# Kernel tuning notes

Measured on AMD Instinct MI355X. Metric: run time of the kernel, lower is better.

The kernel has to match this reference:

```python
import jax, jax.numpy as jnp
import numpy as np
import math

HIDDEN = 1024
Q_SIZE = 1024
KV_SIZE = 1024
OUT_SIZE = 1024
N_HEADS = 16
D_K = HIDDEN // N_HEADS


def setup_inputs() -> dict:
    key = jax.random.key(0)
    ks = jax.random.split(key, 9)
    b, s, t = 8, 2048, 512
    sc = 0.02
    return {
        "hiddens": jax.random.normal(ks[0], (b, s, KV_SIZE), jnp.float32),
        "query_hiddens": jax.random.normal(ks[1], (b, t, Q_SIZE), jnp.float32),
        "mask": jax.random.randint(ks[2], (b, s), 0, 2, jnp.int32),
        "W_q": jax.random.normal(ks[3], (Q_SIZE, HIDDEN), jnp.float32) * sc,
        "b_q": jnp.zeros((HIDDEN,), jnp.float32),
        "W_k": jax.random.normal(ks[4], (KV_SIZE, HIDDEN), jnp.float32) * sc,
        "W_v": jax.random.normal(ks[5], (KV_SIZE, HIDDEN), jnp.float32) * sc,
        "W_o": jax.random.normal(ks[6], (HIDDEN, OUT_SIZE), jnp.float32) * sc,
        "b_o": jnp.zeros((OUT_SIZE,), jnp.float32),
    }


def reference(hiddens, query_hiddens, mask, W_q, b_q, W_k, W_v, W_o, b_o):
    b, t, _ = query_hiddens.shape
    s = hiddens.shape[1]
    # projections (dropout p=0 in eval -> identity)
    Q = (query_hiddens @ W_q + b_q).reshape(b, t, N_HEADS, D_K)
    K = (hiddens @ W_k).reshape(b, s, N_HEADS, D_K)
    V = (hiddens @ W_v).reshape(b, s, N_HEADS, D_K)
    # scores: [b, t, s, h] matching e = (Q*K).sum(-1)/sqrt(d_k)
    e = jnp.einsum('bthd,bshd->btsh', Q, K) / math.sqrt(D_K)
    neg = (1.0 - mask.astype(e.dtype)) * (-1e20)  # [b, s]
    e = e + neg[:, None, :, None]
    a = jax.nn.softmax(e, axis=2)  # softmax over seqlen
    concat = jnp.einsum('btsh,bshd->bthd', a, V).reshape(b, t, HIDDEN)
    context = concat @ W_o + b_o
    return context, a.mean(axis=-1)
```

## Files before the change

### kernel.cpp

```cpp
#include <hip/hip_runtime.h>
#include <hip/hip_bf16.h>

using short8 = __attribute__((ext_vector_type(8))) short;
using f32x4  = __attribute__((ext_vector_type(4))) float;

#define LSK 72

#define GLDS(gptr, lptr) __builtin_amdgcn_global_load_lds( \
    (const __attribute__((address_space(1))) void*)(gptr), \
    (__attribute__((address_space(3))) void*)(lptr), 16, 0, 0)

static __device__ __forceinline__ short f2b(float f) {
    unsigned u = __builtin_bit_cast(unsigned, f);
    unsigned r = (u + 0x7fffu + ((u >> 16) & 1u)) >> 16;
    return (short)r;
}

__global__ void cvt_bf16(const float* __restrict__ in, short* __restrict__ out, int n) {
    int i = (blockIdx.x * 256 + threadIdx.x) * 4;
    if (i >= n) return;
    float4 v = *(const float4*)(in + i);
    short4 o = make_short4(f2b(v.x), f2b(v.y), f2b(v.z), f2b(v.w));
    *(short4*)(out + i) = o;
}

__global__ void cvt_t4(const float* __restrict__ W0, const float* __restrict__ W1,
                       const float* __restrict__ W2, const float* __restrict__ W3,
                       short* __restrict__ Wt0) {
    __shared__ short tile[32][33];
    const float* Ws[4] = {W0, W1, W2, W3};
    const float* W = Ws[blockIdx.z];
    short* Wt = Wt0 + (size_t)blockIdx.z * 1024 * 1024;
    const int K = 1024, N = 1024;
    int n0 = blockIdx.x * 32, k0 = blockIdx.y * 32;
    int tx = threadIdx.x, ty = threadIdx.y;
#pragma unroll
    for (int i = 0; i < 4; i++) {
        int r = ty + i * 8;
        tile[r][tx] = f2b(W[(size_t)(k0 + r) * N + n0 + tx]);
    }
    __syncthreads();
#pragma unroll
    for (int i = 0; i < 4; i++) {
        int r = ty + i * 8;
        Wt[(size_t)(n0 + r) * K + k0 + tx] = tile[tx][r];
    }
}

__global__ __launch_bounds__(512, 2) void gemm256(
    const short* __restrict__ A, const short* __restrict__ Bt,
    short* __restrict__ CK, short* __restrict__ CVt)
{
    __shared__ short As[2][256 * 64];
    __shared__ short Bs[2][256 * 64];
    const int tid = threadIdx.x;
    const int w = tid >> 6, L = tid & 63, quad = L >> 4, l16 = L & 15;
    const int wr = w >> 2, wcn = w & 3;

    const int lin = blockIdx.y * gridDim.x + blockIdx.x;
    const int xcd = lin & 7, idx = lin >> 3;
    const int mPer = gridDim.y >> 3;
    const int my = xcd * mPer + idx / gridDim.x;
    const int nx = idx % gridDim.x;
    const int n0 = nx * 256, m0 = my * 256;

    const int K = 1024;
    const int srow_in = L >> 3;
    const int sgcol   = ((L & 7) ^ srow_in) * 8;

    auto STAGE2 = [&](int buf, int kt, int p) {
#pragma unroll
        for (int j = 0; j < 2; j++) {
            int c = w * 8 + p * 2 + j;
            int k0 = kt * 64;
            if (c < 32) {
                int row = c * 8 + srow_in;
                GLDS(A + (size_t)(m0 + row) * K + k0 + sgcol, &As[buf][c * 512]);
            } else {
                int row = (c - 32) * 8 + srow_in;
                GLDS(Bt + (size_t)(n0 + row) * K + k0 + sgcol, &Bs[buf][(c - 32) * 512]);
            }
        }
    };

    f32x4 acc[2][4][4];
#pragma unroll
    for (int mh = 0; mh < 2; mh++)
#pragma unroll
        for (int mi = 0; mi < 4; mi++)
#pragma unroll
            for (int ni = 0; ni < 4; ni++) acc[mh][mi][ni] = (f32x4){0.f, 0.f, 0.f, 0.f};

#pragma unroll
    for (int p = 0; p < 4; p++) STAGE2(0, 0, p);

    for (int t = 0; t < 16; t++) {
        const int cur = t & 1;
#pragma unroll
        for (int p = 0; p < 4; p++) {
            if (t < 15) STAGE2(cur ^ 1, t + 1, p);
            if (p == 0) {
                if (t < 15) asm volatile("s_waitcnt vmcnt(2)" ::: "memory");
                else        asm volatile("s_waitcnt vmcnt(0)" ::: "memory");
                __builtin_amdgcn_s_barrier();
            }
            const int mh = p & 1, kk = (p >> 1) * 32;
            const int swz = (((kk >> 3) + quad) ^ (l16 & 7)) << 3;
            short8 af[4], bf[4];
#pragma unroll
            for (int mi = 0; mi < 4; mi++)
                af[mi] = *(const short8*)&As[cur][(wr * 128 + mh * 64 + mi * 16 + l16) * 64 + swz];
#pragma unroll
            for (int ni = 0; ni < 4; ni++)
                bf[ni] = *(const short8*)&Bs[cur][(wcn * 64 + ni * 16 + l16) * 64 + swz];
            __builtin_amdgcn_s_setprio(1);
#pragma unroll
            for (int mi = 0; mi < 4; mi++)
#pragma unroll
                for (int ni = 0; ni < 4; ni++)
                    acc[mh][mi][ni] = __builtin_amdgcn_mfma_f32_16x16x32_bf16(af[mi], bf[ni], acc[mh][mi][ni], 0, 0, 0);
            __builtin_amdgcn_s_setprio(0);
            __builtin_amdgcn_s_barrier();
        }
    }

#pragma unroll
    for (int mh = 0; mh < 2; mh++)
#pragma unroll
        for (int ni = 0; ni < 4; ni++) {
            int n = n0 + wcn * 64 + ni * 16 + l16;
#pragma unroll
            for (int mi = 0; mi < 4; mi++)
#pragma unroll
                for (int r = 0; r < 4; r++) {
                    int m = m0 + wr * 128 + mh * 64 + mi * 16 + quad * 4 + r;
                    float v = acc[mh][mi][ni][r];
                    if (n < 1024) CK[(size_t)m * 1024 + n] = f2b(v);
                    else {
                        int h = (n - 1024) >> 6, d = n & 63;
                        int b = m >> 11, s = m & 2047;
                        CVt[(((size_t)b * 16 + h) * 64 + d) * 2048 + s] = f2b(v);
                    }
                }
        }
}

__global__ __launch_bounds__(256) void gemm128(
    const short* __restrict__ A, const short* __restrict__ Bt,
    const float* __restrict__ bias, void* __restrict__ Cout, void* __restrict__ Cout2,
    int M, int mode)
{
    __shared__ short As[2][128 * 64];
    __shared__ short Bs[2][128 * 64];
    const int tid = threadIdx.x;
    const int w = tid >> 6, L = tid & 63, quad = L >> 4, l16 = L & 15;
    const int wr = w >> 1, wc = w & 1;

    const int lin = blockIdx.y * gridDim.x + blockIdx.x;
    const int xcd = lin & 7, idx = lin >> 3;
    const int mPer = gridDim.y >> 3;
    const int my = xcd * mPer + idx / gridDim.x;
    const int nx = idx % gridDim.x;
    const int n0 = nx * 128, m0 = my * 128;

    const int K = 1024;
    const int srow_in = L >> 3;
    const int sgcol   = ((L & 7) ^ (srow_in & 7)) * 8;

    auto STAGE = [&](int buf, int k0) {
#pragma unroll
        for (int j = 0; j < 8; j++) {
            int c = w * 8 + j;
            if (c < 16) {
                int row = c * 8 + srow_in;
                GLDS(A + (size_t)(m0 + row) * K + k0 + sgcol, &As[buf][c * 512]);
            } else {
                int row = (c - 16) * 8 + srow_in;
                GLDS(Bt + (size_t)(n0 + row) * K + k0 + sgcol, &Bs[buf][(c - 16) * 512]);
            }
        }
    };

    f32x4 acc[4][4];
#pragma unroll
    for (int mi = 0; mi < 4; mi++)
#pragma unroll
        for (int ni = 0; ni < 4; ni++) acc[mi][ni] = (f32x4){0.f, 0.f, 0.f, 0.f};

    STAGE(0, 0);
    __syncthreads();

    for (int t = 0; t < 16; t++) {
        const int cur = t & 1;
        if (t < 15) STAGE(cur ^ 1, (t + 1) * 64);
#pragma unroll
        for (int kk = 0; kk < 64; kk += 32) {
            const int swz = (((kk >> 3) + quad) ^ (l16 & 7)) << 3;
            short8 af[4], bf[4];
#pragma unroll
            for (int mi = 0; mi < 4; mi++)
                af[mi] = *(const short8*)&As[cur][(wr * 64 + mi * 16 + l16) * 64 + swz];
#pragma unroll
            for (int ni = 0; ni < 4; ni++)
                bf[ni] = *(const short8*)&Bs[cur][(wc * 64 + ni * 16 + l16) * 64 + swz];
#pragma unroll
            for (int mi = 0; mi < 4; mi++)
#pragma unroll
                for (int ni = 0; ni < 4; ni++)
                    acc[mi][ni] = __builtin_amdgcn_mfma_f32_16x16x32_bf16(af[mi], bf[ni], acc[mi][ni], 0, 0, 0);
        }
        __syncthreads();
    }

#pragma unroll
    for (int ni = 0; ni < 4; ni++) {
        int n = n0 + wc * 64 + ni * 16 + l16;
        float bv = bias ? bias[n] : 0.f;
#pragma unroll
        for (int mi = 0; mi < 4; mi++) {
#pragma unroll
            for (int r = 0; r < 4; r++) {
                int m = m0 + wr * 64 + mi * 16 + quad * 4 + r;
                float v = acc[mi][ni][r] + bv;
                if (mode == 1)      ((float*)Cout)[(size_t)m * 1024 + n] = v;
                else                ((short*)Cout)[(size_t)m * 1024 + n] = f2b(v);
            }
        }
    }
}

__global__ __launch_bounds__(512) void attn_flash(
    const short* __restrict__ Qb, const short* __restrict__ Kb, const short* __restrict__ Vtb,
    const int* __restrict__ mask, short* __restrict__ Cb, float* __restrict__ lse)
{
    __shared__ short Qs[128 * 64];
    __shared__ short Ks[2][128 * 64];
    __shared__ short Vts[2][128 * 64];
    __shared__ short Ps[128 * LSK];
    __shared__ float neg[2][128];
    const int tid = threadIdx.x;
    const int w = tid >> 6, L = tid & 63, quad = L >> 4, l16 = L & 15;
    const int t0 = blockIdx.x * 128, h = blockIdx.y, b = blockIdx.z;
    const int S = 2048, T = 512, H = 1024;
    const int trow = w * 16;
    const int srow = L >> 3;
    const int sg   = ((L & 7) ^ srow) * 8;

    auto STAGE_KV = [&](int buf, int s0) {
#pragma unroll
        for (int j = 0; j < 2; j++) {
            int krow = w * 16 + j * 8 + srow;
            GLDS(Kb + ((size_t)b * S + s0 + krow) * H + h * 64 + sg, &Ks[buf][(w * 16 + j * 8) * 64]);
            int c = w * 2 + j, hf = c >> 3, d0 = (c & 7) * 8;
            GLDS(Vtb + (((size_t)b * 16 + h) * 64 + d0 + srow) * S + s0 + hf * 64 + sg, &Vts[buf][c * 512]);
        }
        if (tid < 128) neg[buf][tid] = mask[(size_t)b * S + s0 + tid] ? 0.f : -1e20f;
    };

#pragma unroll
    for (int j = 0; j < 2; j++) {
        int row = w * 16 + j * 8 + srow;
        GLDS(Qb + ((size_t)b * T + t0 + row) * H + h * 64 + sg, &Qs[(w * 16 + j * 8) * 64]);
    }
    STAGE_KV(0, 0);
    __syncthreads();

    short8 aq[2];
#pragma unroll
    for (int kk = 0; kk < 2; kk++)
        aq[kk] = *(const short8*)&Qs[(trow + l16) * 64 + ((kk * 4 + quad) ^ (l16 & 7)) * 8];

    f32x4 Oacc[4];
#pragma unroll
    for (int nt = 0; nt < 4; nt++) Oacc[nt] = (f32x4){0.f, 0.f, 0.f, 0.f};
    float lsum[4] = {0.f, 0.f, 0.f, 0.f};

    for (int it = 0; it < 16; it++) {
        const int cur = it & 1;
        if (it < 15) STAGE_KV(cur ^ 1, (it + 1) * 128);
#pragma unroll
        for (int hf = 0; hf < 2; hf++) {
            f32x4 sacc[4];
#pragma unroll
            for (int nt = 0; nt < 4; nt++) sacc[nt] = (f32x4){0.f, 0.f, 0.f, 0.f};
#pragma unroll
            for (int kk = 0; kk < 2; kk++) {
#pragma unroll
                for (int nt = 0; nt < 4; nt++) {
                    short8 bf = *(const short8*)&Ks[cur][(hf * 64 + nt * 16 + l16) * 64 + ((kk * 4 + quad) ^ (l16 & 7)) * 8];
                    sacc[nt] = __builtin_amdgcn_mfma_f32_16x16x32_bf16(aq[kk], bf, sacc[nt], 0, 0, 0);
                }
            }
#pragma unroll
            for (int nt = 0; nt < 4; nt++) {
                float ng = neg[cur][hf * 64 + nt * 16 + l16];
#pragma unroll
                for (int r = 0; r < 4; r++) {
                    float e = __expf(fmaf(sacc[nt][r], 0.125f, ng));
                    lsum[r] += e;
                    Ps[(trow + quad * 4 + r) * LSK + nt * 16 + l16] = f2b(e);
                }
            }
#pragma unroll
            for (int kk = 0; kk < 2; kk++) {
                short8 af = *(const short8*)&Ps[(trow + l16) * LSK + kk * 32 + quad * 8];
#pragma unroll
                for (int nt = 0; nt < 4; nt++) {
                    short8 bf = *(const short8*)&Vts[cur][hf * 4096 + (nt * 16 + l16) * 64 + ((kk * 4 + quad) ^ (l16 & 7)) * 8];
                    Oacc[nt] = __builtin_amdgcn_mfma_f32_16x16x32_bf16(af, bf, Oacc[nt], 0, 0, 0);
                }
            }
        }
        __syncthreads();
    }
#pragma unroll
    for (int r = 0; r < 4; r++) {
#pragma unroll
        for (int off = 1; off < 16; off <<= 1)
            lsum[r] += __shfl_xor(lsum[r], off, 64);
    }
#pragma unroll
    for (int r = 0; r < 4; r++) {
        float inv = 1.0f / lsum[r];
        int t = t0 + trow + quad * 4 + r;
#pragma unroll
        for (int nt = 0; nt < 4; nt++) {
            int d = nt * 16 + l16;
            Cb[((size_t)b * T + t) * H + h * 64 + d] = f2b(Oacc[nt][r] * inv);
        }
        if (l16 == 0)
            lse[((size_t)b * 16 + h) * T + t] = __logf(lsum[r]);
    }
}

__global__ __launch_bounds__(256) void attn_amean(
    const short* __restrict__ Qb, const short* __restrict__ Kb,
    const int* __restrict__ mask, const float* __restrict__ lse, float* __restrict__ outA)
{
    __shared__ short Qs[2][64 * 64];
    __shared__ short Ks[2][64 * 64];
    __shared__ float neg[64];
    __shared__ float lss[16 * 64];
    const int tid = threadIdx.x;
    const int w = tid >> 6, L = tid & 63, quad = L >> 4, l16 = L & 15;
    const int s0 = blockIdx.x * 64, t0 = blockIdx.y * 64, b = blockIdx.z;
    const int S = 2048, T = 512, H = 1024;
    const int srow = L >> 3;
    const int sg   = ((L & 7) ^ srow) * 8;

    auto STAGE_QK = [&](int buf, int h) {
#pragma unroll
        for (int j = 0; j < 2; j++) {
            int row = w * 16 + j * 8 + srow;
            GLDS(Qb + ((size_t)b * T + t0 + row) * H + h * 64 + sg, &Qs[buf][(w * 16 + j * 8) * 64]);
            GLDS(Kb + ((size_t)b * S + s0 + row) * H + h * 64 + sg, &Ks[buf][(w * 16 + j * 8) * 64]);
        }
    };

    if (tid < 64) neg[tid] = mask[(size_t)b * S + s0 + tid] ? 0.f : -1e20f;
    for (int i = tid; i < 16 * 64; i += 256) {
        int hh = i >> 6, tt = i & 63;
        lss[i] = lse[((size_t)b * 16 + hh) * T + t0 + tt];
    }
    STAGE_QK(0, 0);
    __syncthreads();

    float am[4][4] = {};
    for (int h = 0; h < 16; h++) {
        const int cur = h & 1;
        if (h < 15) STAGE_QK(cur ^ 1, h + 1);
        short8 aq[2];
#pragma unroll
        for (int kk = 0; kk < 2; kk++)
            aq[kk] = *(const short8*)&Qs[cur][(w * 16 + l16) * 64 + ((kk * 4 + quad) ^ (l16 & 7)) * 8];
        f32x4 sacc[4];
#pragma unroll
        for (int nt = 0; nt < 4; nt++) sacc[nt] = (f32x4){0.f, 0.f, 0.f, 0.f};
#pragma unroll
        for (int kk = 0; kk < 2; kk++) {
#pragma unroll
            for (int nt = 0; nt < 4; nt++) {
                short8 bf = *(const short8*)&Ks[cur][(nt * 16 + l16) * 64 + ((kk * 4 + quad) ^ (l16 & 7)) * 8];
                sacc[nt] = __builtin_amdgcn_mfma_f32_16x16x32_bf16(aq[kk], bf, sacc[nt], 0, 0, 0);
            }
        }
#pragma unroll
        for (int nt = 0; nt < 4; nt++) {
            float ng = neg[nt * 16 + l16];
#pragma unroll
            for (int r = 0; r < 4; r++) {
                int trow = w * 16 + quad * 4 + r;
                am[nt][r] += __expf(fmaf(sacc[nt][r], 0.125f, ng - lss[h * 64 + trow]));
            }
        }
        __syncthreads();
    }
#pragma unroll
    for (int r = 0; r < 4; r++) {
        int t = t0 + w * 16 + quad * 4 + r;
#pragma unroll
        for (int nt = 0; nt < 4; nt++) {
            int s = s0 + nt * 16 + l16;
            outA[((size_t)b * T + t) * S + s] = am[nt][r] * 0.0625f;
        }
    }
}

extern "C" void kernel_launch(void* const* d_in, const int* in_sizes, int n_in,
                              void* d_out, int out_size, void* d_ws, size_t ws_size,
                              hipStream_t stream) {
    const float* hiddens = (const float*)d_in[0];
    const float* query   = (const float*)d_in[1];
    const int*   mask    = (const int*)d_in[2];
    const float* W_q = (const float*)d_in[3];
    const float* b_q = (const float*)d_in[4];
    const float* W_k = (const float*)d_in[5];
    const float* W_v = (const float*)d_in[6];
    const float* W_o = (const float*)d_in[7];
    const float* b_o = (const float*)d_in[8];
    float* out = (float*)d_out;

    constexpr size_t N_H  = 8UL * 2048 * 1024;
    constexpr size_t N_QH = 8UL * 512 * 1024;
    constexpr size_t N_W  = 1024UL * 1024;
    char* ws = (char*)d_ws;
    short* Hb   = (short*)(ws);
    short* QHb  = (short*)(ws + N_H * 2);
    short* Wqt  = (short*)(ws + N_H * 2 + N_QH * 2);
    short* Wkt  = Wqt + N_W;
    short* Wvt  = Wkt + N_W;
    short* Wot  = Wvt + N_W;
    short* Qb   = Wot + N_W;
    short* Kb   = Qb + N_QH;
    short* Vtb  = Kb + N_H;
    short* Cb   = Vtb + N_H;
    float* lseP = (float*)(Cb + N_QH);

    cvt_bf16<<<16384, 256, 0, stream>>>(hiddens, Hb, (int)N_H);
    cvt_bf16<<<4096, 256, 0, stream>>>(query, QHb, (int)N_QH);
    cvt_t4<<<dim3(32, 32, 4), dim3(32, 8), 0, stream>>>(W_q, W_k, W_v, W_o, Wqt);

    gemm128<<<dim3(8, 32), 256, 0, stream>>>(QHb, Wqt, b_q, Qb, nullptr, 4096, 0);
    gemm256<<<dim3(8, 64), 512, 0, stream>>>(Hb, Wkt, Kb, Vtb);

    attn_flash<<<dim3(4, 16, 8), 512, 0, stream>>>(Qb, Kb, Vtb, mask, Cb, lseP);

    gemm128<<<dim3(8, 32), 256, 0, stream>>>(Cb, Wot, b_o, out, nullptr, 4096, 1);
    attn_amean<<<dim3(32, 8, 8), 256, 0, stream>>>(Qb, Kb, mask, lseP, out + N_QH);
}
```

Baseline: 433.7 us.

## Restructure GEMM and attention pipelines with one-barrier-per-tile waitcnt sync and preloaded mask

The 256 GEMM now issues all next-tile global-to-LDS loads at once, waits with a vmcnt and a single barrier per K tile, and reorders fragment loads so B fragments are reused across both M halves. Its launch bound drops to one block per SIMD group. The 128 GEMM and both attention kernels replace __syncthreads with explicit vmcnt-based top and end barriers so prefetch overlaps compute. The flash kernel loads the whole mask row into LDS once via 4-byte direct loads instead of per-tile scalar writes. The aim is fewer barriers and better latency hiding, at the cost of hand-tuned wait counts that must match the number of outstanding loads, and a possible occupancy change in the 256 GEMM.

Result: no change. 437.3 us (+0.8%).

```diff
diff --git a/kernel.cpp b/kernel.cpp
--- a/kernel.cpp
+++ b/kernel.cpp
@@ -9,6 +9,20 @@
 #define GLDS(gptr, lptr) __builtin_amdgcn_global_load_lds( \
     (const __attribute__((address_space(1))) void*)(gptr), \
     (__attribute__((address_space(3))) void*)(lptr), 16, 0, 0)
+
+#define GLDS4(gptr, lptr) __builtin_amdgcn_global_load_lds( \
+    (const __attribute__((address_space(1))) void*)(gptr), \
+    (__attribute__((address_space(3))) void*)(lptr), 4, 0, 0)
+
+#define TOPSYNC_V(n_lit) do { \
+    asm volatile("s_waitcnt vmcnt(" #n_lit ")" ::: "memory"); \
+    __builtin_amdgcn_s_barrier(); \
+    __builtin_amdgcn_sched_barrier(0); \
+} while (0)
+#define ENDSYNC() do { \
+    __builtin_amdgcn_sched_barrier(0); \
+    __builtin_amdgcn_s_barrier(); \
+} while (0)
 
 static __device__ __forceinline__ short f2b(float f) {
     unsigned u = __builtin_bit_cast(unsigned, f);
@@ -47,7 +61,7 @@
     }
 }
 
-__global__ __launch_bounds__(512, 2) void gemm256(
+__global__ __launch_bounds__(512, 1) void gemm256(
     const short* __restrict__ A, const short* __restrict__ Bt,
     short* __restrict__ CK, short* __restrict__ CVt)
 {
@@ -68,11 +82,11 @@
     const int srow_in = L >> 3;
     const int sgcol   = ((L & 7) ^ srow_in) * 8;
 
-    auto STAGE2 = [&](int buf, int kt, int p) {
-#pragma unroll
-        for (int j = 0; j < 2; j++) {
-            int c = w * 8 + p * 2 + j;
-            int k0 = kt * 64;
+    auto STAGE_ALL = [&](int buf, int kt) {
+        const int k0 = kt * 64;
+#pragma unroll
+        for (int j = 0; j < 8; j++) {
+            int c = w * 8 + j;
             if (c < 32) {
                 int row = c * 8 + srow_in;
                 GLDS(A + (size_t)(m0 + row) * K + k0 + sgcol, &As[buf][c * 512]);
@@ -91,37 +105,39 @@
 #pragma unroll
             for (int ni = 0; ni < 4; ni++) acc[mh][mi][ni] = (f32x4){0.f, 0.f, 0.f, 0.f};
 
-#pragma unroll
-    for (int p = 0; p < 4; p++) STAGE2(0, 0, p);
+    STAGE_ALL(0, 0);
 
     for (int t = 0; t < 16; t++) {
         const int cur = t & 1;
-#pragma unroll
-        for (int p = 0; p < 4; p++) {
-            if (t < 15) STAGE2(cur ^ 1, t + 1, p);
-            if (p == 0) {
-                if (t < 15) asm volatile("s_waitcnt vmcnt(2)" ::: "memory");
-                else        asm volatile("s_waitcnt vmcnt(0)" ::: "memory");
-                __builtin_amdgcn_s_barrier();
-            }
-            const int mh = p & 1, kk = (p >> 1) * 32;
-            const int swz = (((kk >> 3) + quad) ^ (l16 & 7)) << 3;
-            short8 af[4], bf[4];
-#pragma unroll
-            for (int mi = 0; mi < 4; mi++)
-                af[mi] = *(const short8*)&As[cur][(wr * 128 + mh * 64 + mi * 16 + l16) * 64 + swz];
+        if (t < 15) {
+            STAGE_ALL(cur ^ 1, t + 1);
+            TOPSYNC_V(8);
+        } else {
+            TOPSYNC_V(0);
+        }
+#pragma unroll
+        for (int ks = 0; ks < 2; ks++) {
+            const int swz = (((ks * 4) + quad) ^ (l16 & 7)) << 3;
+            short8 bf[4];
 #pragma unroll
             for (int ni = 0; ni < 4; ni++)
                 bf[ni] = *(const short8*)&Bs[cur][(wcn * 64 + ni * 16 + l16) * 64 + swz];
-            __builtin_amdgcn_s_setprio(1);
-#pragma unroll
-            for (int mi = 0; mi < 4; mi++)
-#pragma unroll
-                for (int ni = 0; ni < 4; ni++)
-                    acc[mh][mi][ni] = __builtin_amdgcn_mfma_f32_16x16x32_bf16(af[mi], bf[ni], acc[mh][mi][ni], 0, 0, 0);
-            __builtin_amdgcn_s_setprio(0);
-            __builtin_amdgcn_s_barrier();
-        }
+#pragma unroll
+            for (int mh = 0; mh < 2; mh++) {
+                short8 af[4];
+#pragma unroll
+                for (int mi = 0; mi < 4; mi++)
+                    af[mi] = *(const short8*)&As[cur][(wr * 128 + mh * 64 + mi * 16 + l16) * 64 + swz];
+                __builtin_amdgcn_s_setprio(1);
+#pragma unroll
+                for (int mi = 0; mi < 4; mi++)
+#pragma unroll
+                    for (int ni = 0; ni < 4; ni++)
+                        acc[mh][mi][ni] = __builtin_amdgcn_mfma_f32_16x16x32_bf16(af[mi], bf[ni], acc[mh][mi][ni], 0, 0, 0);
+                __builtin_amdgcn_s_setprio(0);
+            }
+        }
+        ENDSYNC();
     }
 
 #pragma unroll
@@ -147,7 +163,7 @@
 
 __global__ __launch_bounds__(256) void gemm128(
     const short* __restrict__ A, const short* __restrict__ Bt,
-    const float* __restrict__ bias, void* __restrict__ Cout, void* __restrict__ Cout2,
+    const float* __restrict__ bias, void* __restrict__ Cout,
     int M, int mode)
 {
     __shared__ short As[2][128 * 64];
@@ -188,11 +204,15 @@
         for (int ni = 0; ni < 4; ni++) acc[mi][ni] = (f32x4){0.f, 0.f, 0.f, 0.f};
 
     STAGE(0, 0);
-    __syncthreads();
 
     for (int t = 0; t < 16; t++) {
         const int cur = t & 1;
-        if (t < 15) STAGE(cur ^ 1, (t + 1) * 64);
+        if (t < 15) {
+            STAGE(cur ^ 1, (t + 1) * 64);
+            TOPSYNC_V(8);
+        } else {
+            TOPSYNC_V(0);
+        }
 #pragma unroll
         for (int kk = 0; kk < 64; kk += 32) {
             const int swz = (((kk >> 3) + quad) ^ (l16 & 7)) << 3;
@@ -209,7 +229,7 @@
                 for (int ni = 0; ni < 4; ni++)
                     acc[mi][ni] = __builtin_amdgcn_mfma_f32_16x16x32_bf16(af[mi], bf[ni], acc[mi][ni], 0, 0, 0);
         }
-        __syncthreads();
+        ENDSYNC();
     }
 
 #pragma unroll
@@ -237,7 +257,7 @@
     __shared__ short Ks[2][128 * 64];
     __shared__ short Vts[2][128 * 64];
     __shared__ short Ps[128 * LSK];
-    __shared__ float neg[2][128];
+    __shared__ int   negi[2048];
     const int tid = threadIdx.x;
     const int w = tid >> 6, L = tid & 63, quad = L >> 4, l16 = L & 15;
     const int t0 = blockIdx.x * 128, h = blockIdx.y, b = blockIdx.z;
@@ -254,7 +274,6 @@
             int c = w * 2 + j, hf = c >> 3, d0 = (c & 7) * 8;
             GLDS(Vtb + (((size_t)b * 16 + h) * 64 + d0 + srow) * S + s0 + hf * 64 + sg, &Vts[buf][c * 512]);
         }
-        if (tid < 128) neg[buf][tid] = mask[(size_t)b * S + s0 + tid] ? 0.f : -1e20f;
     };
 
 #pragma unroll
@@ -262,6 +281,9 @@
         int row = w * 16 + j * 8 + srow;
         GLDS(Qb + ((size_t)b * T + t0 + row) * H + h * 64 + sg, &Qs[(w * 16 + j * 8) * 64]);
     }
+#pragma unroll
+    for (int r = 0; r < 4; r++)
+        GLDS4(mask + (size_t)b * S + r * 512 + w * 64 + L, &negi[r * 512 + w * 64]);
     STAGE_KV(0, 0);
     __syncthreads();
 
@@ -277,7 +299,12 @@
 
     for (int it = 0; it < 16; it++) {
         const int cur = it & 1;
-        if (it < 15) STAGE_KV(cur ^ 1, (it + 1) * 128);
+        if (it < 15) {
+            STAGE_KV(cur ^ 1, (it + 1) * 128);
+            TOPSYNC_V(4);
+        } else {
+            TOPSYNC_V(0);
+        }
 #pragma unroll
         for (int hf = 0; hf < 2; hf++) {
             f32x4 sacc[4];
@@ -293,7 +320,7 @@
             }
 #pragma unroll
             for (int nt = 0; nt < 4; nt++) {
-                float ng = neg[cur][hf * 64 + nt * 16 + l16];
+                float ng = negi[it * 128 + hf * 64 + nt * 16 + l16] ? 0.f : -1e20f;
 #pragma unroll
                 for (int r = 0; r < 4; r++) {
                     float e = __expf(fmaf(sacc[nt][r], 0.125f, ng));
@@ -311,7 +338,7 @@
                 }
             }
         }
-        __syncthreads();
+        ENDSYNC();
     }
 #pragma unroll
     for (int r = 0; r < 4; r++) {
@@ -368,7 +395,12 @@
     float am[4][4] = {};
     for (int h = 0; h < 16; h++) {
         const int cur = h & 1;
-        if (h < 15) STAGE_QK(cur ^ 1, h + 1);
+        if (h < 15) {
+            STAGE_QK(cur ^ 1, h + 1);
+            TOPSYNC_V(4);
+        } else {
+            TOPSYNC_V(0);
+        }
         short8 aq[2];
 #pragma unroll
         for (int kk = 0; kk < 2; kk++)
@@ -393,7 +425,7 @@
                 am[nt][r] += __expf(fmaf(sacc[nt][r], 0.125f, ng - lss[h * 64 + trow]));
             }
         }
-        __syncthreads();
+        ENDSYNC();
     }
 #pragma unroll
     for (int r = 0; r < 4; r++) {
@@ -440,11 +472,11 @@
     cvt_bf16<<<4096, 256, 0, stream>>>(query, QHb, (int)N_QH);
     cvt_t4<<<dim3(32, 32, 4), dim3(32, 8), 0, stream>>>(W_q, W_k, W_v, W_o, Wqt);
 
-    gemm128<<<dim3(8, 32), 256, 0, stream>>>(QHb, Wqt, b_q, Qb, nullptr, 4096, 0);
+    gemm128<<<dim3(8, 32), 256, 0, stream>>>(QHb, Wqt, b_q, Qb, 4096, 0);
     gemm256<<<dim3(8, 64), 512, 0, stream>>>(Hb, Wkt, Kb, Vtb);
 
     attn_flash<<<dim3(4, 16, 8), 512, 0, stream>>>(Qb, Kb, Vtb, mask, Cb, lseP);
 
-    gemm128<<<dim3(8, 32), 256, 0, stream>>>(Cb, Wot, b_o, out, nullptr, 4096, 1);
+    gemm128<<<dim3(8, 32), 256, 0, stream>>>(Cb, Wot, b_o, out, 4096, 1);
     attn_amean<<<dim3(32, 8, 8), 256, 0, stream>>>(Qb, Kb, mask, lseP, out + N_QH);
 }
```
